# Kernel optimization log

Measured on AMD Instinct MI355X. Metric: run time of the kernel, lower is better.

Reference implementation:

```python
import jax, jax.numpy as jnp
import numpy as np

B, T, C, H = 2, 2048, 1024, 16
D = C // H  # head dim = 64
EPS = 1e-6  # kernel adds 1e-6 to softmax denominator


def setup_inputs() -> dict:
    key = jax.random.key(0)
    k1, k2, k3, k4, k5 = jax.random.split(key, 5)
    s = 1.0 / np.sqrt(C)
    return {
        "x": jax.random.normal(k1, (B, T, C), dtype=jnp.float32),
        "w_attn": jax.random.normal(k2, (3 * C, C), dtype=jnp.float32) * s,
        "b_attn": jax.random.normal(k3, (3 * C,), dtype=jnp.float32) * 0.02,
        "w_proj": jax.random.normal(k4, (C, C), dtype=jnp.float32) * s,
        "b_proj": jax.random.normal(k5, (C,), dtype=jnp.float32) * 0.02,
    }


def reference(x, w_attn, b_attn, w_proj, b_proj):
    b, t, c = x.shape
    qkv = x @ w_attn.T + b_attn                      # [B,T,3C]
    q, k, v = jnp.split(qkv, 3, axis=2)
    # [B,T,C] -> [B,H,T,D]
    q = q.reshape(b, t, H, D).transpose(0, 2, 1, 3)
    k = k.reshape(b, t, H, D).transpose(0, 2, 1, 3)
    v = v.reshape(b, t, H, D).transpose(0, 2, 1, 3)
    scale = 1.0 / np.sqrt(D)
    att = jnp.einsum("bhid,bhjd->bhij", q, k) * scale  # [B,H,T,T]
    causal = jnp.tril(jnp.ones((t, t), dtype=bool))
    att = jnp.where(causal, att, -jnp.inf)
    # softmax matching the HIP kernel: denom has +1e-6
    m = jnp.max(att, axis=-1, keepdims=True)
    e = jnp.exp(att - m)                             # masked entries -> 0
    p = e / (jnp.sum(e, axis=-1, keepdims=True) + EPS)
    y = jnp.einsum("bhij,bhjd->bhid", p, v)          # [B,H,T,D]
    y = y.transpose(0, 2, 1, 3).reshape(b, t, c)     # [B,T,C]
    return y @ w_proj.T + b_proj
```

## Files before the change

### kernel.cpp

```cpp
#include <hip/hip_runtime.h>

#define B_ 2
#define T_ 2048
#define C_ 1024
#define H_ 16
#define D_ 64

typedef __bf16 bf16x8 __attribute__((ext_vector_type(8)));
typedef float f32x4 __attribute__((ext_vector_type(4)));

__device__ __forceinline__ unsigned short f2bf(float f) {
  unsigned u = __float_as_uint(f);
  unsigned r = (u + 0x7fffu + ((u >> 16) & 1u)) >> 16;
  return (unsigned short)r;
}

#define NX 1048576
#define NWA 786432
#define NWP 262144
__global__ __launch_bounds__(256) void convert_all(
    const float* __restrict__ x, const float* __restrict__ wa,
    const float* __restrict__ wp, unsigned short* __restrict__ xb,
    unsigned short* __restrict__ wab, unsigned short* __restrict__ wpb) {
  int i = blockIdx.x * 256 + threadIdx.x;
  const float* s; unsigned short* d; int j;
  if (i < NX)            { s = x;  d = xb;  j = i; }
  else if (i < NX + NWA) { s = wa; d = wab; j = i - NX; }
  else                   { s = wp; d = wpb; j = i - NX - NWA; }
  float4 v = ((const float4*)s)[j];
  ushort4 u;
  u.x = f2bf(v.x); u.y = f2bf(v.y); u.z = f2bf(v.z); u.w = f2bf(v.w);
  ((ushort4*)d)[j] = u;
}

__global__ __launch_bounds__(256) void gemm_bt(
    const unsigned short* __restrict__ A,
    const unsigned short* __restrict__ Bm,
    const float* __restrict__ bias,
    int M, int N, int K, int mode,
    float* __restrict__ outf,
    unsigned short* __restrict__ qb,
    unsigned short* __restrict__ kb,
    unsigned short* __restrict__ vb) {
  __shared__ unsigned short As[128 * 64];
  __shared__ unsigned short Bs[128 * 64];

  const int tid  = threadIdx.x;
  const int lane = tid & 63;
  const int wave = tid >> 6;
  const int quad = lane >> 4;
  const int l16  = lane & 15;
  const int q4   = quad * 4;

  const int bm = blockIdx.y * 128;
  const int bn = blockIdx.x * 128;
  const int wm = (wave >> 1) * 64;
  const int wn = (wave & 1) * 64;

  f32x4 acc[4][4] = {};

  const int srow8 = lane >> 3;
  const int scol  = ((lane & 7) ^ srow8) * 8;
  const int srow  = wave * 8 + srow8;

  for (int k0 = 0; k0 < K; k0 += 64) {
#pragma unroll
    for (int c = 0; c < 4; ++c) {
      const int r = c * 32 + srow;
      const unsigned short* ga = A  + (size_t)(bm + r) * K + (k0 + scol);
      const unsigned short* gb = Bm + (size_t)(bn + r) * K + (k0 + scol);
      unsigned short* la = &As[(c * 32 + wave * 8) * 64];
      unsigned short* lb = &Bs[(c * 32 + wave * 8) * 64];
      __builtin_amdgcn_global_load_lds(
          (__attribute__((address_space(1))) unsigned int*)ga,
          (__attribute__((address_space(3))) unsigned int*)la, 16, 0, 0);
      __builtin_amdgcn_global_load_lds(
          (__attribute__((address_space(1))) unsigned int*)gb,
          (__attribute__((address_space(3))) unsigned int*)lb, 16, 0, 0);
    }
    __syncthreads();
#pragma unroll
    for (int ks = 0; ks < 2; ++ks) {
      bf16x8 af[4], bfr[4];
#pragma unroll
      for (int i = 0; i < 4; ++i)
        af[i] = *(const bf16x8*)&As[(wm + i * 16 + l16) * 64 +
                                    (((ks * 4 + quad) ^ (l16 & 7)) * 8)];
#pragma unroll
      for (int j = 0; j < 4; ++j)
        bfr[j] = *(const bf16x8*)&Bs[(wn + j * 16 + l16) * 64 +
                                     (((ks * 4 + quad) ^ (l16 & 7)) * 8)];
#pragma unroll
      for (int i = 0; i < 4; ++i)
#pragma unroll
        for (int j = 0; j < 4; ++j)
          acc[i][j] = __builtin_amdgcn_mfma_f32_16x16x32_bf16(af[i], bfr[j], acc[i][j], 0, 0, 0);
    }
    __syncthreads();
  }

#pragma unroll
  for (int j = 0; j < 4; ++j) {
    const int gn = bn + wn + j * 16 + l16;
    const float bv = bias[gn];
    if (mode == 0) {
#pragma unroll
      for (int i = 0; i < 4; ++i)
#pragma unroll
        for (int r = 0; r < 4; ++r) {
          const int gm = bm + wm + i * 16 + q4 + r;
          outf[(size_t)gm * N + gn] = acc[i][j][r] + bv;
        }
    } else {
      const int which = gn >> 10;
      const int cc = gn & 1023;
      const int h = cc >> 6, d = cc & 63;
      if (which == 2) {
#pragma unroll
        for (int i = 0; i < 4; ++i) {
          const int gm0 = bm + wm + i * 16 + q4;
          const int b = gm0 >> 11, t0 = gm0 & 2047;
          ushort4 u;
          u.x = f2bf(acc[i][j][0] + bv);
          u.y = f2bf(acc[i][j][1] + bv);
          u.z = f2bf(acc[i][j][2] + bv);
          u.w = f2bf(acc[i][j][3] + bv);
          *(ushort4*)&vb[(((size_t)(b * H_ + h) * D_) + d) * T_ + t0] = u;
        }
      } else {
        const float sc = (which == 0) ? 0.125f : 1.0f;
        unsigned short* dst = (which == 0) ? qb : kb;
#pragma unroll
        for (int i = 0; i < 4; ++i)
#pragma unroll
          for (int r = 0; r < 4; ++r) {
            const int gm = bm + wm + i * 16 + q4 + r;
            const int b = gm >> 11, t = gm & 2047;
            dst[(((size_t)(b * H_ + h) * T_) + t) * D_ + d] = f2bf((acc[i][j][r] + bv) * sc);
          }
      }
    }
  }
}

__global__ __launch_bounds__(256, 2) void attn_mfma(
    const unsigned short* __restrict__ Qb,
    const unsigned short* __restrict__ Kb,
    const unsigned short* __restrict__ Vtg,
    unsigned short* __restrict__ Yb,
    unsigned short* __restrict__ op,
    float* __restrict__ lp) {
  __shared__ unsigned short Ks[64 * 64];
  __shared__ unsigned short Vt[64 * 64];
  __shared__ unsigned short Pw[4][32 * 64];

  const int tid  = threadIdx.x;
  const int lane = tid & 63;
  const int wave = tid >> 6;
  const int quad = lane >> 4;
  const int l16  = lane & 15;
  const int q4   = quad * 4;
  const int sw   = (l16 & 7);

  const int id = blockIdx.x;
  const int bh = id / 40;
  const int w  = id - bh * 40;
  int qt, chunk, nsplits;
  if (w < 4)       { qt = w;                 chunk = 0;            nsplits = 1; }
  else if (w < 12) { qt = 4 + ((w - 4) >> 1); chunk = (w - 4) & 1;  nsplits = 2; }
  else if (w < 24) { qt = 8 + (w - 12) / 3;  chunk = (w - 12) % 3; nsplits = 3; }
  else             { qt = 12 + ((w - 24) >> 2); chunk = (w - 24) & 3; nsplits = 4; }

  const int tiles_total = 2 * qt + 2;
  const int tpc = (tiles_total + nsplits - 1) / nsplits;
  const int t0 = chunk * tpc;
  const int t1 = min(t0 + tpc, tiles_total);

  const int b = bh >> 4, h = bh & 15;
  const size_t base = (size_t)bh * T_ * D_;
  const int wq = qt * 128 + wave * 32;
  const int wt1 = min(t1, (wq + 95) >> 6);

  bf16x8 qf[2][2];
#pragma unroll
  for (int nt = 0; nt < 2; ++nt)
#pragma unroll
    for (int ks = 0; ks < 2; ++ks)
      qf[nt][ks] = *(const bf16x8*)(Qb + base + (size_t)(wq + nt * 16 + l16) * 64 +
                                    ks * 32 + quad * 8);

  f32x4 o[4][2] = {};
  float l2[2] = {0.f, 0.f};

  const int srow8 = lane >> 3;
  const int satom = ((lane & 7) ^ srow8) * 8;

  for (int kt = t0; kt < t1; ++kt) {
    const int kt0 = kt * 64;
    __syncthreads();
#pragma unroll
    for (int c = 0; c < 2; ++c) {
      const int row = wave * 16 + c * 8 + srow8;
      const unsigned short* gk = Kb  + base + (size_t)(kt0 + row) * 64 + satom;
      const unsigned short* gv = Vtg + base + (size_t)row * T_ + kt0 + satom;
      unsigned short* lk = &Ks[(wave * 16 + c * 8) * 64];
      unsigned short* lv = &Vt[(wave * 16 + c * 8) * 64];
      __builtin_amdgcn_global_load_lds(
          (__attribute__((address_space(1))) unsigned int*)gk,
          (__attribute__((address_space(3))) unsigned int*)lk, 16, 0, 0);
      __builtin_amdgcn_global_load_lds(
          (__attribute__((address_space(1))) unsigned int*)gv,
          (__attribute__((address_space(3))) unsigned int*)lv, 16, 0, 0);
    }
    __syncthreads();

    if (kt < wt1) {
      f32x4 s[4][2] = {};
#pragma unroll
      for (int ks = 0; ks < 2; ++ks) {
        bf16x8 kf[4];
#pragma unroll
        for (int mt = 0; mt < 4; ++mt)
          kf[mt] = *(const bf16x8*)&Ks[(mt * 16 + l16) * 64 +
                                       (((ks * 4 + quad) ^ sw) * 8)];
#pragma unroll
        for (int mt = 0; mt < 4; ++mt)
#pragma unroll
          for (int nt = 0; nt < 2; ++nt)
            s[mt][nt] = __builtin_amdgcn_mfma_f32_16x16x32_bf16(kf[mt], qf[nt][ks],
                                                                s[mt][nt], 0, 0, 0);
      }
      if (kt0 + 63 > wq) {
#pragma unroll
        for (int mt = 0; mt < 4; ++mt)
#pragma unroll
          for (int nt = 0; nt < 2; ++nt)
#pragma unroll
            for (int r = 0; r < 4; ++r)
              if (kt0 + mt * 16 + q4 + r > wq + nt * 16 + l16) s[mt][nt][r] = -1e30f;
      }
#pragma unroll
      for (int nt = 0; nt < 2; ++nt) {
        float ps = 0.f;
#pragma unroll
        for (int mt = 0; mt < 4; ++mt) {
          float p0 = __expf(s[mt][nt][0]);
          float p1 = __expf(s[mt][nt][1]);
          float p2 = __expf(s[mt][nt][2]);
          float p3 = __expf(s[mt][nt][3]);
          ps += (p0 + p1) + (p2 + p3);
          unsigned lo = __builtin_amdgcn_perm(__float_as_uint(p1) + 0x8000u,
                                              __float_as_uint(p0) + 0x8000u,
                                              0x07060302u);
          unsigned hi = __builtin_amdgcn_perm(__float_as_uint(p3) + 0x8000u,
                                              __float_as_uint(p2) + 0x8000u,
                                              0x07060302u);
          uint2 pk; pk.x = lo; pk.y = hi;
          const int atom = (2 * mt + (quad >> 1)) ^ sw;
          *(uint2*)&Pw[wave][(nt * 16 + l16) * 64 + atom * 8 + (quad & 1) * 4] = pk;
        }
        l2[nt] += ps;
      }
#pragma unroll
      for (int ks = 0; ks < 2; ++ks) {
        bf16x8 vf[4], pf[2];
#pragma unroll
        for (int dt = 0; dt < 4; ++dt)
          vf[dt] = *(const bf16x8*)&Vt[(dt * 16 + l16) * 64 +
                                       (((ks * 4 + quad) ^ sw) * 8)];
#pragma unroll
        for (int nt = 0; nt < 2; ++nt)
          pf[nt] = *(const bf16x8*)&Pw[wave][(nt * 16 + l16) * 64 +
                                            (((ks * 4 + quad) ^ sw) * 8)];
#pragma unroll
        for (int dt = 0; dt < 4; ++dt)
#pragma unroll
          for (int nt = 0; nt < 2; ++nt)
            o[dt][nt] = __builtin_amdgcn_mfma_f32_16x16x32_bf16(vf[dt], pf[nt],
                                                                o[dt][nt], 0, 0, 0);
      }
    }
  }

#pragma unroll
  for (int nt = 0; nt < 2; ++nt) {
    float l = l2[nt];
    l += __shfl_xor(l, 16);
    l += __shfl_xor(l, 32);
    const int qloc = wave * 32 + nt * 16 + l16;
    if (nsplits == 1) {
      const float inv = 1.f / (l + 1e-6f);
      const int q = qt * 128 + qloc;
#pragma unroll
      for (int dt = 0; dt < 4; ++dt) {
        ushort4 u;
        u.x = f2bf(o[dt][nt][0] * inv);
        u.y = f2bf(o[dt][nt][1] * inv);
        u.z = f2bf(o[dt][nt][2] * inv);
        u.w = f2bf(o[dt][nt][3] * inv);
        *(ushort4*)&Yb[((size_t)(b * T_ + q)) * C_ + h * 64 + dt * 16 + q4] = u;
      }
    } else {
      if (quad == 0) lp[(size_t)id * 128 + qloc] = l;
#pragma unroll
      for (int dt = 0; dt < 4; ++dt) {
        ushort4 u;
        u.x = f2bf(o[dt][nt][0]);
        u.y = f2bf(o[dt][nt][1]);
        u.z = f2bf(o[dt][nt][2]);
        u.w = f2bf(o[dt][nt][3]);
        *(ushort4*)&op[(size_t)id * 8192 + (size_t)qloc * 64 + dt * 16 + q4] = u;
      }
    }
  }
}

__global__ __launch_bounds__(256) void attn_combine(
    const unsigned short* __restrict__ op, const float* __restrict__ lp,
    unsigned short* __restrict__ Yb) {
  const int cb = blockIdx.x;
  const int bh = cb / 12;
  const int qi = cb - bh * 12;
  const int qt = 4 + qi;
  int nsplits, pfx;
  if (qt < 8)       { nsplits = 2; pfx = 4 + 2 * (qt - 4); }
  else if (qt < 12) { nsplits = 3; pfx = 12 + 3 * (qt - 8); }
  else              { nsplits = 4; pfx = 24 + 4 * (qt - 12); }
  const int slot0 = bh * 40 + pfx;

  const int t = threadIdx.x;
  const int qloc = t >> 1;
  const int d0 = (t & 1) * 32;

  float l = 1e-6f;
  float acc[32];
#pragma unroll
  for (int i = 0; i < 32; ++i) acc[i] = 0.f;
  for (int s = 0; s < nsplits; ++s) {
    l += lp[(size_t)(slot0 + s) * 128 + qloc];
    const uint4* src = (const uint4*)(op + (size_t)(slot0 + s) * 8192 +
                                      (size_t)qloc * 64 + d0);
#pragma unroll
    for (int c = 0; c < 4; ++c) {
      uint4 v = src[c];
      acc[c*8+0] += __uint_as_float(v.x << 16);
      acc[c*8+1] += __uint_as_float(v.x & 0xffff0000u);
      acc[c*8+2] += __uint_as_float(v.y << 16);
      acc[c*8+3] += __uint_as_float(v.y & 0xffff0000u);
      acc[c*8+4] += __uint_as_float(v.z << 16);
      acc[c*8+5] += __uint_as_float(v.z & 0xffff0000u);
      acc[c*8+6] += __uint_as_float(v.w << 16);
      acc[c*8+7] += __uint_as_float(v.w & 0xffff0000u);
    }
  }
  const float inv = 1.f / l;
  const int b = bh >> 4, h = bh & 15;
  const int q = qt * 128 + qloc;
  uint4* dst = (uint4*)(Yb + ((size_t)(b * T_ + q)) * C_ + h * 64 + d0);
#pragma unroll
  for (int c = 0; c < 4; ++c) {
    uint4 v;
    v.x = (unsigned)f2bf(acc[c*8+0] * inv) | ((unsigned)f2bf(acc[c*8+1] * inv) << 16);
    v.y = (unsigned)f2bf(acc[c*8+2] * inv) | ((unsigned)f2bf(acc[c*8+3] * inv) << 16);
    v.z = (unsigned)f2bf(acc[c*8+4] * inv) | ((unsigned)f2bf(acc[c*8+5] * inv) << 16);
    v.w = (unsigned)f2bf(acc[c*8+6] * inv) | ((unsigned)f2bf(acc[c*8+7] * inv) << 16);
    dst[c] = v;
  }
}

extern "C" void kernel_launch(void* const* d_in, const int* in_sizes, int n_in,
                              void* d_out, int out_size, void* d_ws, size_t ws_size,
                              hipStream_t stream) {
  const float* x      = (const float*)d_in[0];
  const float* w_attn = (const float*)d_in[1];
  const float* b_attn = (const float*)d_in[2];
  const float* w_proj = (const float*)d_in[3];
  const float* b_proj = (const float*)d_in[4];
  float* out = (float*)d_out;

  char* ws = (char*)d_ws;
  unsigned short* xb  = (unsigned short*)ws;  ws += (size_t)4096 * 1024 * 2;
  unsigned short* wab = (unsigned short*)ws;  ws += (size_t)3072 * 1024 * 2;
  unsigned short* wpb = (unsigned short*)ws;  ws += (size_t)1024 * 1024 * 2;
  unsigned short* qb  = (unsigned short*)ws;  ws += (size_t)B_ * H_ * T_ * D_ * 2;
  unsigned short* kb  = (unsigned short*)ws;  ws += (size_t)B_ * H_ * T_ * D_ * 2;
  unsigned short* vb  = (unsigned short*)ws;  ws += (size_t)B_ * H_ * T_ * D_ * 2;
  unsigned short* yb  = (unsigned short*)ws;  ws += (size_t)4096 * 1024 * 2;
  unsigned short* op  = (unsigned short*)ws;  ws += (size_t)1280 * 128 * 64 * 2;
  float*          lp  = (float*)ws;           ws += (size_t)1280 * 128 * 4;
  (void)ws_size; (void)in_sizes; (void)n_in; (void)out_size;

  convert_all<<<8192, 256, 0, stream>>>(x, w_attn, w_proj, xb, wab, wpb);

  gemm_bt<<<dim3(24, 32), 256, 0, stream>>>(xb, wab, b_attn, 4096, 3072, 1024, 1,
                                            nullptr, qb, kb, vb);
  attn_mfma<<<1280, 256, 0, stream>>>(qb, kb, vb, yb, op, lp);
  attn_combine<<<384, 256, 0, stream>>>(op, lp, yb);
  gemm_bt<<<dim3(8, 32), 256, 0, stream>>>(yb, wpb, b_proj, 4096, 1024, 1024, 0,
                                           out, nullptr, nullptr, nullptr);
}
```

Measured before the change: 184.2 us.

## Double-buffer K/V tiles in attention and use hardware exp2 and bf16 pack

The attention kernel now keeps two LDS buffers for K and V. It issues the async global-to-LDS load for the next key tile before computing on the current one, which drops one barrier per iteration and hides load latency. The log2(e) factor is folded into the Q scale so softmax can use the raw v_exp_f32 instruction. The manual bf16 rounding via perm is replaced by v_cvt_pk_bf16_f32, and s_setprio is raised around the MFMA blocks. The costs are double the K/V LDS footprint, which may affect occupancy, and reliance on the barrier's implicit vmcnt wait for correctness.

New measurement: 185.8 us. Within noise of the previous version (+0.9%).

```diff
diff --git a/kernel.cpp b/kernel.cpp
--- a/kernel.cpp
+++ b/kernel.cpp
@@ -13,6 +13,12 @@
   unsigned u = __float_as_uint(f);
   unsigned r = (u + 0x7fffu + ((u >> 16) & 1u)) >> 16;
   return (unsigned short)r;
+}
+
+__device__ __forceinline__ float exp2_hw(float x) {
+  float r;
+  asm("v_exp_f32 %0, %1" : "=v"(r) : "v"(x));
+  return r;
 }
 
 #define NX 1048576
@@ -128,7 +134,7 @@
           *(ushort4*)&vb[(((size_t)(b * H_ + h) * D_) + d) * T_ + t0] = u;
         }
       } else {
-        const float sc = (which == 0) ? 0.125f : 1.0f;
+        const float sc = (which == 0) ? 0.18033688011112042f : 1.0f;
         unsigned short* dst = (which == 0) ? qb : kb;
 #pragma unroll
         for (int i = 0; i < 4; ++i)
@@ -150,8 +156,8 @@
     unsigned short* __restrict__ Yb,
     unsigned short* __restrict__ op,
     float* __restrict__ lp) {
-  __shared__ unsigned short Ks[64 * 64];
-  __shared__ unsigned short Vt[64 * 64];
+  __shared__ unsigned short Ks[2][64 * 64];
+  __shared__ unsigned short Vt[2][64 * 64];
   __shared__ unsigned short Pw[4][32 * 64];
 
   const int tid  = threadIdx.x;
@@ -195,24 +201,32 @@
   const int srow8 = lane >> 3;
   const int satom = ((lane & 7) ^ srow8) * 8;
 
+#define STAGE_KV(KT, BI)                                                       \
+  do {                                                                         \
+    const int kt0s = (KT) * 64;                                                \
+    _Pragma("unroll")                                                          \
+    for (int c = 0; c < 2; ++c) {                                              \
+      const int row = wave * 16 + c * 8 + srow8;                               \
+      const unsigned short* gk = Kb + base + (size_t)(kt0s + row) * 64 + satom;\
+      const unsigned short* gv = Vtg + base + (size_t)row * T_ + kt0s + satom; \
+      unsigned short* lk = &Ks[BI][(wave * 16 + c * 8) * 64];                  \
+      unsigned short* lv = &Vt[BI][(wave * 16 + c * 8) * 64];                  \
+      __builtin_amdgcn_global_load_lds(                                        \
+          (__attribute__((address_space(1))) unsigned int*)gk,                 \
+          (__attribute__((address_space(3))) unsigned int*)lk, 16, 0, 0);      \
+      __builtin_amdgcn_global_load_lds(                                        \
+          (__attribute__((address_space(1))) unsigned int*)gv,                 \
+          (__attribute__((address_space(3))) unsigned int*)lv, 16, 0, 0);      \
+    }                                                                          \
+  } while (0)
+
+  STAGE_KV(t0, 0);
+  int cur = 0;
+
   for (int kt = t0; kt < t1; ++kt) {
     const int kt0 = kt * 64;
     __syncthreads();
-#pragma unroll
-    for (int c = 0; c < 2; ++c) {
-      const int row = wave * 16 + c * 8 + srow8;
-      const unsigned short* gk = Kb  + base + (size_t)(kt0 + row) * 64 + satom;
-      const unsigned short* gv = Vtg + base + (size_t)row * T_ + kt0 + satom;
-      unsigned short* lk = &Ks[(wave * 16 + c * 8) * 64];
-      unsigned short* lv = &Vt[(wave * 16 + c * 8) * 64];
-      __builtin_amdgcn_global_load_lds(
-          (__attribute__((address_space(1))) unsigned int*)gk,
-          (__attribute__((address_space(3))) unsigned int*)lk, 16, 0, 0);
-      __builtin_amdgcn_global_load_lds(
-          (__attribute__((address_space(1))) unsigned int*)gv,
-          (__attribute__((address_space(3))) unsigned int*)lv, 16, 0, 0);
-    }
-    __syncthreads();
+    if (kt + 1 < t1) STAGE_KV(kt + 1, cur ^ 1);
 
     if (kt < wt1) {
       f32x4 s[4][2] = {};
@@ -221,14 +235,16 @@
         bf16x8 kf[4];
 #pragma unroll
         for (int mt = 0; mt < 4; ++mt)
-          kf[mt] = *(const bf16x8*)&Ks[(mt * 16 + l16) * 64 +
-                                       (((ks * 4 + quad) ^ sw) * 8)];
+          kf[mt] = *(const bf16x8*)&Ks[cur][(mt * 16 + l16) * 64 +
+                                           (((ks * 4 + quad) ^ sw) * 8)];
+        __builtin_amdgcn_s_setprio(1);
 #pragma unroll
         for (int mt = 0; mt < 4; ++mt)
 #pragma unroll
           for (int nt = 0; nt < 2; ++nt)
             s[mt][nt] = __builtin_amdgcn_mfma_f32_16x16x32_bf16(kf[mt], qf[nt][ks],
                                                                 s[mt][nt], 0, 0, 0);
+        __builtin_amdgcn_s_setprio(0);
       }
       if (kt0 + 63 > wq) {
 #pragma unroll
@@ -244,17 +260,14 @@
         float ps = 0.f;
 #pragma unroll
         for (int mt = 0; mt < 4; ++mt) {
-          float p0 = __expf(s[mt][nt][0]);
-          float p1 = __expf(s[mt][nt][1]);
-          float p2 = __expf(s[mt][nt][2]);
-          float p3 = __expf(s[mt][nt][3]);
+          float p0 = exp2_hw(s[mt][nt][0]);
+          float p1 = exp2_hw(s[mt][nt][1]);
+          float p2 = exp2_hw(s[mt][nt][2]);
+          float p3 = exp2_hw(s[mt][nt][3]);
           ps += (p0 + p1) + (p2 + p3);
-          unsigned lo = __builtin_amdgcn_perm(__float_as_uint(p1) + 0x8000u,
-                                              __float_as_uint(p0) + 0x8000u,
-                                              0x07060302u);
-          unsigned hi = __builtin_amdgcn_perm(__float_as_uint(p3) + 0x8000u,
-                                              __float_as_uint(p2) + 0x8000u,
-                                              0x07060302u);
+          unsigned lo, hi;
+          asm("v_cvt_pk_bf16_f32 %0, %1, %2" : "=v"(lo) : "v"(p0), "v"(p1));
+          asm("v_cvt_pk_bf16_f32 %0, %1, %2" : "=v"(hi) : "v"(p2), "v"(p3));
           uint2 pk; pk.x = lo; pk.y = hi;
           const int atom = (2 * mt + (quad >> 1)) ^ sw;
           *(uint2*)&Pw[wave][(nt * 16 + l16) * 64 + atom * 8 + (quad & 1) * 4] = pk;
@@ -266,21 +279,25 @@
         bf16x8 vf[4], pf[2];
 #pragma unroll
         for (int dt = 0; dt < 4; ++dt)
-          vf[dt] = *(const bf16x8*)&Vt[(dt * 16 + l16) * 64 +
-                                       (((ks * 4 + quad) ^ sw) * 8)];
+          vf[dt] = *(const bf16x8*)&Vt[cur][(dt * 16 + l16) * 64 +
+                                           (((ks * 4 + quad) ^ sw) * 8)];
 #pragma unroll
         for (int nt = 0; nt < 2; ++nt)
           pf[nt] = *(const bf16x8*)&Pw[wave][(nt * 16 + l16) * 64 +
                                             (((ks * 4 + quad) ^ sw) * 8)];
+        __builtin_amdgcn_s_setprio(1);
 #pragma unroll
         for (int dt = 0; dt < 4; ++dt)
 #pragma unroll
           for (int nt = 0; nt < 2; ++nt)
             o[dt][nt] = __builtin_amdgcn_mfma_f32_16x16x32_bf16(vf[dt], pf[nt],
                                                                 o[dt][nt], 0, 0, 0);
-      }
-    }
-  }
+        __builtin_amdgcn_s_setprio(0);
+      }
+    }
+    cur ^= 1;
+  }
+#undef STAGE_KV
 
 #pragma unroll
   for (int nt = 0; nt < 2; ++nt) {
```
